# Kernel optimization log

Hardware: AMD Instinct MI355X
Metric: run time of the kernel (lower is better)

Reference implementation:

```python
import jax, jax.numpy as jnp
import numpy as np

R = 8            # receptive_field (hardcoded r=8 in GridProcessing call)
MARGIN = 0.6     # TripletLoss(margin=0.6)
EPS = 1e-8       # F.cosine_similarity eps


def _mine_cords(B, FH, FW):
    """Replicates GridProcessing._prepare for an identity flow field
    G[b, y, x] = ((x + 0.5) / W, (y + 0.5) / H):
    at every cell center, G_xmin = x, G_xmax = x + 1, both inside bounds, and
    [x // r, (x + 1) // r + 1) = {ix}, so the positive window collapses to the
    cell itself -> anchor_cord == positive_cord == (b, ix, iy) for every cell.
    (clip(0, 31) is benign since FH = FW = 32.)
    Negative cords from _prepare are discarded by forward(), so not produced."""
    bs, ys, xs = np.meshgrid(np.arange(B), np.arange(FH), np.arange(FW), indexing='ij')
    idx = np.stack([bs, xs, ys], axis=-1).reshape(-1, 3).astype(np.int32)  # rows: (b, x, y)
    return idx, idx.copy()


def setup_inputs() -> dict:
    key = jax.random.key(0)
    B, C, FH, FW = 16, 1024, 32, 32
    k1, k2 = jax.random.split(key)
    sketch = jax.random.normal(k1, (B, C, FH, FW), dtype=jnp.float32)
    ref = jax.random.normal(k2, (B, C, FH, FW), dtype=jnp.float32)
    a_idx, p_idx = _mine_cords(B, FH, FW)
    return {
        'sketch_query_vectors': sketch,
        'ref_key_vectors': ref,
        'anchor_idx': jnp.asarray(a_idx),
        'positive_idx': jnp.asarray(p_idx),
    }


def reference(sketch_query_vectors, ref_key_vectors, anchor_idx, positive_idx):
    B, C, FH, FW = sketch_query_vectors.shape
    HW = FH * FW
    N = anchor_idx.shape[0]
    na = N // B  # anchor rows are ordered by batch index, na anchors per image

    ax = anchor_idx[:, 1].reshape(B, na)
    ay = anchor_idx[:, 2].reshape(B, na)
    # anchor = sketch[b, :, y, x]  -> (B, na, C)
    a = sketch_query_vectors[jnp.arange(B)[:, None], :, ay, ax]

    # ref_fs.view(c, h*w).permute(1, 0): row-major flatten, flat id = y*W + x
    ref_flat = ref_key_vectors.reshape(B, C, HW).transpose(0, 2, 1)  # (B, HW, C)

    # cosine similarity of every anchor vs every ref position (per batch)
    dots = jnp.einsum('bnc,bmc->bnm', a, ref_flat)          # (B, na, HW)
    a_n = jnp.linalg.norm(a, axis=-1)                        # (B, na)
    r_n = jnp.linalg.norm(ref_flat, axis=-1)                 # (B, HW)
    sim = dots / jnp.maximum(a_n[:, :, None] * r_n[:, None, :], EPS)

    # get_negative_ids: argsort(dist)[:3] -> 3 LOWEST cosine positions;
    # loss uses sum of the 3 anchor-negative cosines (broadcasted cosine sum)
    neg_sum = -jnp.sum(jax.lax.top_k(-sim, 3)[0], axis=-1)   # (B, na)

    # cos(anchor, positive) is just sim at the positive's flat position
    pos_flat = (positive_idx[:, 2] * FW + positive_idx[:, 1]).reshape(B, na)
    cos_ap = jnp.take_along_axis(sim, pos_flat[:, :, None], axis=2)[..., 0]

    # (1 - cos_ap) - (1 - neg_sum) + margin, relu, mean over the single triplet
    losses = jax.nn.relu(neg_sum - cos_ap + MARGIN)          # (B, na)
    return jnp.sum(losses) / (1e-6 + N)
```

## Files before the change

### kernel.cpp

```cpp
#include <hip/hip_runtime.h>
#include <hip/hip_bf16.h>
#include <stdint.h>

#define BATCH 16
#define CDIM  1024
#define FWID  32
#define HW    1024
#define NA    1024
#define NTOT  (BATCH*NA)
#define NCHUNK 16
#define MARGIN 0.6f

typedef __bf16 bf16x8 __attribute__((ext_vector_type(8)));
typedef float  f32x4  __attribute__((ext_vector_type(4)));
typedef unsigned short us4 __attribute__((ext_vector_type(4)));
typedef unsigned short us8 __attribute__((ext_vector_type(8)));
typedef float  f4     __attribute__((ext_vector_type(4)));

template<int OFF>
__device__ __forceinline__ us4 tr_read(uint32_t addr){
  us4 r;
  asm volatile("ds_read_b64_tr_b16 %0, %1 offset:%2" : "=v"(r) : "v"(addr), "n"(OFF));
  return r;
}

__device__ __forceinline__ void gload16(const unsigned short* g, unsigned short* l){
  __builtin_amdgcn_global_load_lds((const __attribute__((address_space(1))) void*)g,
                                   (__attribute__((address_space(3))) void*)l, 16, 0, 0);
}

union FragU  { us4 h[2]; bf16x8 v; };
union FragU8 { us8 u;    bf16x8 v; };

__device__ __forceinline__ void ins3(float& a, float& b, float& c, float v){
  if (v < c){
    c = v;
    if (c < b){ float t=b; b=c; c=t;
      if (b < a){ t=a; a=b; b=t; }
    }
  }
}

#define MFMA __builtin_amdgcn_mfma_f32_16x16x32_bf16

__global__ __launch_bounds__(256)
void convert_transpose(const float* __restrict__ S, const float* __restrict__ R,
                       unsigned short* __restrict__ tS, unsigned short* __restrict__ tR,
                       float* __restrict__ pnorm){
  const int blk = blockIdx.x;
  const int e   = blk >> 11;
  const int b   = (blk >> 7) & 15;
  const int hwT = (blk >> 3) & 15;
  const int cT  = blk & 7;
  const float* src = (e ? R : S) + (size_t)b*CDIM*HW;
  unsigned short* dst = (e ? tR : tS) + (size_t)b*HW*CDIM;

  const int t   = threadIdx.x;
  const int cj  = t & 15;
  const int hwg = t >> 4;
  const int hw0 = hwT*64 + hwg*4;
  const int c0  = cT*128 + cj*8;

  f4 col[8];
  #pragma unroll
  for (int i = 0; i < 8; ++i)
    col[i] = *(const f4*)&src[(size_t)(c0 + i)*HW + hw0];

  float sq0=0.f, sq1=0.f, sq2=0.f, sq3=0.f;
  #pragma unroll
  for (int j = 0; j < 4; ++j){
    us8 pk;
    float sq = 0.f;
    #pragma unroll
    for (int i = 0; i < 8; ++i){
      __hip_bfloat16 h = __float2bfloat16(col[i][j]);
      pk[i] = __builtin_bit_cast(unsigned short, h);
      const float g = __bfloat162float(h);
      sq = fmaf(g, g, sq);
    }
    *(us8*)&dst[(size_t)(hw0 + j)*CDIM + c0] = pk;
    if (j==0) sq0=sq; else if (j==1) sq1=sq; else if (j==2) sq2=sq; else sq3=sq;
  }
  #pragma unroll
  for (int m = 1; m < 16; m <<= 1){
    sq0 += __shfl_xor(sq0, m);
    sq1 += __shfl_xor(sq1, m);
    sq2 += __shfl_xor(sq2, m);
    sq3 += __shfl_xor(sq3, m);
  }
  if (cj == 0){
    f4 o = {sq0, sq1, sq2, sq3};
    *(f4*)&pnorm[((size_t)(e*16 + b)*8 + cT)*HW + hw0] = o;
  }
}

__global__ __launch_bounds__(256)
void norm_reduce(const float* __restrict__ pnorm, float* __restrict__ snorm){
  const int eb = blockIdx.x;
  const int t  = threadIdx.x;
  #pragma unroll
  for (int r = 0; r < 4; ++r){
    const int hw = r*256 + t;
    float a = 0.f;
    #pragma unroll
    for (int ct = 0; ct < 8; ++ct)
      a += pnorm[((size_t)eb*8 + ct)*HW + hw];
    snorm[(size_t)eb*HW + hw] = sqrtf(a);
  }
}

__global__ __launch_bounds__(512, 2)
void fused_gemm_top3_v5(const unsigned short* __restrict__ tS,
                        const unsigned short* __restrict__ tR,
                        const float* __restrict__ snorm,
                        const int*   __restrict__ anchor,
                        const int*   __restrict__ posidx,
                        float* __restrict__ wtop,
                        float* __restrict__ wpos)
{
  __shared__ unsigned short stage[49152];
  __shared__ int   p_lds[256], q_lds[256];
  __shared__ float nAs[256], nBs[256];

  const int t = threadIdx.x;
  const uint32_t bid = blockIdx.x;
  const uint32_t L = (bid & 7u)*32u + (bid >> 3);
  const int b  = L >> 4;
  const int ni = (L >> 2) & 3;
  const int mi = L & 3;

  const unsigned short* SbT = tS + (size_t)b*HW*CDIM;
  const unsigned short* RbT = tR + (size_t)b*HW*CDIM;

  if (t < 256){
    const int n_g = ni*256 + t;
    const int* ap = anchor + (size_t)(b*NA + n_g)*3;
    const int* pp = posidx + (size_t)(b*NA + n_g)*3;
    const int pv = ap[2]*FWID + ap[1];
    p_lds[t] = pv;
    q_lds[t] = pp[2]*FWID + pp[1];
    nAs[t] = 1.0f / snorm[(size_t)b*HW + pv];
  } else {
    nBs[t-256] = 1.0f / snorm[(size_t)(BATCH + b)*HW + mi*256 + (t-256)];
  }
  __syncthreads();

  const int l  = t & 63;
  const int w  = t >> 6;
  const int wr = w >> 2, wc = w & 3;

  const int gkc = (l&3) ^ ((l>>3)&3);
  const int r0  = w*32 + (l>>2);
  const int r1  = r0 + 16;
  const unsigned short* gA0 = SbT + (size_t)p_lds[r0]*CDIM + gkc*8;
  const unsigned short* gA1 = SbT + (size_t)p_lds[r1]*CDIM + gkc*8;
  const unsigned short* gB0 = RbT + (size_t)(mi*256 + r0)*CDIM + gkc*8;
  const unsigned short* gB1 = RbT + (size_t)(mi*256 + r1)*CDIM + gkc*8;
  unsigned short* lA = &stage[w*1024];
  unsigned short* lB = &stage[24576 + w*1024];

  const int fbase = (l&15)*32 + (((l>>4) ^ ((l>>1)&3))*8);
  const int abase = wr*4096 + fbase;
  const int bbase = 24576 + wc*2048 + fbase;

  f32x4 acc[8][4];
  #pragma unroll
  for (int i=0;i<8;i++){
    #pragma unroll
    for (int j=0;j<4;j++){ f32x4 z = {0.f,0.f,0.f,0.f}; acc[i][j] = z; }
  }

  auto stage_fn = [&](int bo, int kt){
    const int ko = kt*32;
    gload16(gA0 + ko, lA + bo);
    gload16(gA1 + ko, lA + bo + 512);
    gload16(gB0 + ko, lB + bo);
    gload16(gB1 + ko, lB + bo + 512);
  };

  auto compute = [&](int bo){
    FragU8 Bf[4], Af[8];
    #pragma unroll
    for (int fb=0; fb<4; ++fb) Bf[fb].u = *(const us8*)&stage[bbase + bo + fb*512];
    #pragma unroll
    for (int fa=0; fa<8; ++fa) Af[fa].u = *(const us8*)&stage[abase + bo + fa*512];
    #pragma unroll
    for (int fa=0; fa<8; ++fa){
      #pragma unroll
      for (int fb=0; fb<4; ++fb)
        acc[fa][fb] = MFMA(Af[fa].v, Bf[fb].v, acc[fa][fb], 0,0,0);
    }
  };

  stage_fn(0, 0);
  stage_fn(8192, 1);
  int oc = 0, on = 8192, on2 = 16384;
  for (int kt = 0; kt < 32; ++kt){
    if (kt < 31) asm volatile("s_waitcnt vmcnt(4)" ::: "memory");
    else         asm volatile("s_waitcnt vmcnt(0)" ::: "memory");
    asm volatile("s_waitcnt lgkmcnt(0)" ::: "memory");
    __builtin_amdgcn_s_barrier();
    if (kt < 30) stage_fn(on2, kt+2);
    compute(oc);
    const int tmp = oc; oc = on; on = on2; on2 = tmp;
  }

  __syncthreads();

  float* tls = (float*)&stage[0] + (size_t)w*1152;

  float rinv[4];
  #pragma unroll
  for (int fb=0; fb<4; ++fb) rinv[fb] = nBs[wc*64 + fb*16 + (l&15)];

  #pragma unroll
  for (int fa=0; fa<8; ++fa){
    #pragma unroll
    for (int r=0; r<4; ++r){
      const int rg    = (l>>4)*4 + r;
      const int row_l = wr*128 + fa*16 + rg;
      const float ain = nAs[row_l];
      const float v0 = acc[fa][0][r] * ain * rinv[0];
      const float v1 = acc[fa][1][r] * ain * rinv[1];
      const float v2 = acc[fa][2][r] * ain * rinv[2];
      const float v3 = acc[fa][3][r] * ain * rinv[3];

      const int n_g = ni*256 + row_l;
      const int q   = q_lds[row_l];
      const int ql  = q - (mi*256 + wc*64);
      if (ql >= 0 && ql < 64 && (ql & 15) == (l & 15)){
        const int sel = ql >> 4;
        const float pv = sel==0 ? v0 : sel==1 ? v1 : sel==2 ? v2 : v3;
        wpos[b*NA + n_g] = pv;
      }

      float x=1e30f, y=1e30f, z=1e30f;
      ins3(x,y,z,v0); ins3(x,y,z,v1); ins3(x,y,z,v2); ins3(x,y,z,v3);
      f4 tr = {x, y, z, 0.f};
      *(f4*)(tls + (rg*17 + (l&15))*4) = tr;
    }
    asm volatile("s_waitcnt lgkmcnt(0)" ::: "memory");
    __builtin_amdgcn_sched_barrier(0);

    {
      const int rr = l >> 2;
      const float* rbp = tls + (rr*17 + (l&3)*4)*4;
      const f4 t0 = *(const f4*)(rbp);
      const f4 t1 = *(const f4*)(rbp + 4);
      const f4 t2 = *(const f4*)(rbp + 8);
      const f4 t3 = *(const f4*)(rbp + 12);
      float x = t0[0], y = t0[1], z = t0[2];
      ins3(x,y,z,t1[0]); ins3(x,y,z,t1[1]); ins3(x,y,z,t1[2]);
      ins3(x,y,z,t2[0]); ins3(x,y,z,t2[1]); ins3(x,y,z,t2[2]);
      ins3(x,y,z,t3[0]); ins3(x,y,z,t3[1]); ins3(x,y,z,t3[2]);
      #pragma unroll
      for (int m=1; m<4; m<<=1){
        const float ox = __shfl_xor(x, m);
        const float oy = __shfl_xor(y, m);
        const float oz = __shfl_xor(z, m);
        ins3(x,y,z,ox); ins3(x,y,z,oy); ins3(x,y,z,oz);
      }
      if ((l & 3) == 0){
        const int n_g = ni*256 + wr*128 + fa*16 + rr;
        float* dst = wtop + ((size_t)(b*NA + n_g)*NCHUNK + (mi*4 + wc))*3;
        dst[0]=x; dst[1]=y; dst[2]=z;
      }
    }
    asm volatile("s_waitcnt lgkmcnt(0)" ::: "memory");
    __builtin_amdgcn_sched_barrier(0);
  }
}

__global__ __launch_bounds__(256)
void fused_gemm_top3_v1(const float* __restrict__ sketch,
                        const float* __restrict__ refk,
                        const int*   __restrict__ anchor,
                        const int*   __restrict__ posidx,
                        float* __restrict__ wtop,
                        float* __restrict__ wpos)
{
  __shared__ union {
    unsigned short stage[16384];
    struct { float nA[16][128]; float nB[16][128]; } nrm;
  } sh;
  __shared__ int   p_lds[128];
  __shared__ float nA2[128], nB2[128];

  const int t = threadIdx.x;
  const uint32_t bid = blockIdx.x;
  const uint32_t L = (bid & 7u)*128u + (bid >> 3);
  const int b  = L >> 6;
  const int ni = (L >> 3) & 7;
  const int mi = L & 7;

  const float* Sb = sketch + (size_t)b*CDIM*HW;
  const float* Rb = refk   + (size_t)b*CDIM*HW;

  if (t < 128){
    const int n_g = ni*128 + t;
    const int* ap = anchor + (size_t)(b*NA + n_g)*3;
    p_lds[t] = ap[2]*FWID + ap[1];
  }
  __syncthreads();
  const int p0 = p_lds[0];
  int okf = 1;
  if (t < 128) okf = (p_lds[t] == p0 + t);
  const int contig = __syncthreads_and(okf);

  const int colg = (t & 15)*8;
  const int rowg = t >> 4;
  const int mbase = mi*128;

  const int l  = t & 63;
  const int w  = t >> 6;
  const int wr = w >> 1, wc = w & 1;
  const uint32_t sh_base = (uint32_t)(uintptr_t)&sh.stage[0];
  const uint32_t laneA = ((uint32_t)(l>>4))*2048u + (uint32_t)wr*512u + (uint32_t)(l&15)*8u;
  const uint32_t laneB = ((uint32_t)(l>>4))*2048u + (uint32_t)wc*512u + (uint32_t)(l&15)*8u;
  const int off0 = ((rowg>>2)*8 + (colg>>4))*64 + (rowg&3)*16 + (colg&15);

  f32x4 acc[4][4];
  #pragma unroll
  for (int i=0;i<4;i++){
    #pragma unroll
    for (int j=0;j<4;j++){ f32x4 z = {0.f,0.f,0.f,0.f}; acc[i][j] = z; }
  }

  float sqA[8] = {0,0,0,0,0,0,0,0};
  float sqB[8] = {0,0,0,0,0,0,0,0};
  f4 ra[4], rb[4];

  auto load_tile = [&](int kt){
    const int c0 = kt*32 + rowg;
    const float* SA = Sb + (size_t)c0*HW;
    const float* RB = Rb + (size_t)c0*HW + mbase + colg;
    if (contig){
      const float* pA = SA + p0 + colg;
      ra[0] = *(const f4*)(pA);
      ra[1] = *(const f4*)(pA + 4);
      ra[2] = *(const f4*)(pA + 16*HW);
      ra[3] = *(const f4*)(pA + 16*HW + 4);
    } else {
      float* raf = (float*)ra;
      #pragma unroll
      for (int i=0;i<8;i++){
        const int pc = p_lds[colg + i];
        raf[i]   = SA[pc];
        raf[8+i] = SA[16*HW + pc];
      }
    }
    rb[0] = *(const f4*)(RB);
    rb[1] = *(const f4*)(RB + 4);
    rb[2] = *(const f4*)(RB + 16*HW);
    rb[3] = *(const f4*)(RB + 16*HW + 4);
  };

  auto cvt_store = [&](int buf){
    const float* raf = (const float*)ra;
    const float* rbf = (const float*)rb;
    us8 pk;
    #pragma unroll
    for (int i=0;i<8;i++){
      __hip_bfloat16 h = __float2bfloat16(raf[i]);
      pk[i] = __builtin_bit_cast(unsigned short, h);
      const float g = __bfloat162float(h);
      sqA[i] = fmaf(g, g, sqA[i]);
    }
    *(us8*)&sh.stage[buf*4096 + off0] = pk;
    #pragma unroll
    for (int i=0;i<8;i++){
      __hip_bfloat16 h = __float2bfloat16(raf[8+i]);
      pk[i] = __builtin_bit_cast(unsigned short, h);
      const float g = __bfloat162float(h);
      sqA[i] = fmaf(g, g, sqA[i]);
    }
    *(us8*)&sh.stage[buf*4096 + off0 + 2048] = pk;
    #pragma unroll
    for (int i=0;i<8;i++){
      __hip_bfloat16 h = __float2bfloat16(rbf[i]);
      pk[i] = __builtin_bit_cast(unsigned short, h);
      const float g = __bfloat162float(h);
      sqB[i] = fmaf(g, g, sqB[i]);
    }
    *(us8*)&sh.stage[8192 + buf*4096 + off0] = pk;
    #pragma unroll
    for (int i=0;i<8;i++){
      __hip_bfloat16 h = __float2bfloat16(rbf[8+i]);
      pk[i] = __builtin_bit_cast(unsigned short, h);
      const float g = __bfloat162float(h);
      sqB[i] = fmaf(g, g, sqB[i]);
    }
    *(us8*)&sh.stage[8192 + buf*4096 + off0 + 2048] = pk;
  };

  auto compute = [&](int buf){
    const uint32_t aaddr = sh_base + (uint32_t)buf*8192u + laneA;
    const uint32_t baddr = sh_base + 16384u + (uint32_t)buf*8192u + laneB;
    FragU A0,A1,A2,A3,B0,B1,B2,B3;
    A0.h[0]=tr_read<0>(aaddr);    A0.h[1]=tr_read<1024>(aaddr);
    A1.h[0]=tr_read<128>(aaddr);  A1.h[1]=tr_read<1152>(aaddr);
    A2.h[0]=tr_read<256>(aaddr);  A2.h[1]=tr_read<1280>(aaddr);
    A3.h[0]=tr_read<384>(aaddr);  A3.h[1]=tr_read<1408>(aaddr);
    B0.h[0]=tr_read<0>(baddr);    B0.h[1]=tr_read<1024>(baddr);
    B1.h[0]=tr_read<128>(baddr);  B1.h[1]=tr_read<1152>(baddr);
    B2.h[0]=tr_read<256>(baddr);  B2.h[1]=tr_read<1280>(baddr);
    B3.h[0]=tr_read<384>(baddr);  B3.h[1]=tr_read<1408>(baddr);
    asm volatile("s_waitcnt lgkmcnt(0)" ::: "memory");
    __builtin_amdgcn_sched_barrier(0);
    acc[0][0]=MFMA(A0.v,B0.v,acc[0][0],0,0,0);
    acc[0][1]=MFMA(A0.v,B1.v,acc[0][1],0,0,0);
    acc[0][2]=MFMA(A0.v,B2.v,acc[0][2],0,0,0);
    acc[0][3]=MFMA(A0.v,B3.v,acc[0][3],0,0,0);
    acc[1][0]=MFMA(A1.v,B0.v,acc[1][0],0,0,0);
    acc[1][1]=MFMA(A1.v,B1.v,acc[1][1],0,0,0);
    acc[1][2]=MFMA(A1.v,B2.v,acc[1][2],0,0,0);
    acc[1][3]=MFMA(A1.v,B3.v,acc[1][3],0,0,0);
    acc[2][0]=MFMA(A2.v,B0.v,acc[2][0],0,0,0);
    acc[2][1]=MFMA(A2.v,B1.v,acc[2][1],0,0,0);
    acc[2][2]=MFMA(A2.v,B2.v,acc[2][2],0,0,0);
    acc[2][3]=MFMA(A2.v,B3.v,acc[2][3],0,0,0);
    acc[3][0]=MFMA(A3.v,B0.v,acc[3][0],0,0,0);
    acc[3][1]=MFMA(A3.v,B1.v,acc[3][1],0,0,0);
    acc[3][2]=MFMA(A3.v,B2.v,acc[3][2],0,0,0);
    acc[3][3]=MFMA(A3.v,B3.v,acc[3][3],0,0,0);
  };

  load_tile(0);
  cvt_store(0);
  __syncthreads();
  int buf = 0;
  for (int kt = 0; kt < 32; ++kt){
    if (kt < 31) load_tile(kt+1);
    compute(buf);
    if (kt < 31) cvt_store(buf^1);
    __syncthreads();
    buf ^= 1;
  }

  #pragma unroll
  for (int i=0;i<8;i++) sh.nrm.nA[rowg][colg+i] = sqA[i];
  #pragma unroll
  for (int i=0;i<8;i++) sh.nrm.nB[rowg][colg+i] = sqB[i];
  __syncthreads();
  if (t < 128){
    float s = 0.f;
    #pragma unroll
    for (int r=0;r<16;r++) s += sh.nrm.nA[r][t];
    nA2[t] = s;
  } else {
    const int c2 = t - 128;
    float s = 0.f;
    #pragma unroll
    for (int r=0;r<16;r++) s += sh.nrm.nB[r][c2];
    nB2[c2] = s;
  }
  __syncthreads();

  float rncol[4];
  #pragma unroll
  for (int nf=0;nf<4;nf++) rncol[nf] = sqrtf(nB2[wc*64 + nf*16 + (l&15)]);

  #pragma unroll
  for (int mf=0; mf<4; ++mf){
    #pragma unroll
    for (int r=0; r<4; ++r){
      const int row_l = wr*64 + mf*16 + (l>>4)*4 + r;
      const int n_g   = ni*128 + row_l;
      const float an  = sqrtf(nA2[row_l]);
      const float v0 = acc[mf][0][r] / fmaxf(an*rncol[0], 1e-8f);
      const float v1 = acc[mf][1][r] / fmaxf(an*rncol[1], 1e-8f);
      const float v2 = acc[mf][2][r] / fmaxf(an*rncol[2], 1e-8f);
      const float v3 = acc[mf][3][r] / fmaxf(an*rncol[3], 1e-8f);

      const int* pp = posidx + (size_t)(b*NA + n_g)*3;
      const int q  = pp[2]*FWID + pp[1];
      const int ql = q - (mbase + wc*64);
      if (ql >= 0 && ql < 64 && (ql & 15) == (l & 15)){
        const int sel = ql >> 4;
        const float pv = sel==0 ? v0 : sel==1 ? v1 : sel==2 ? v2 : v3;
        wpos[b*NA + n_g] = pv;
      }

      float x=1e30f, y=1e30f, z=1e30f;
      ins3(x,y,z,v0); ins3(x,y,z,v1); ins3(x,y,z,v2); ins3(x,y,z,v3);
      #pragma unroll
      for (int m=1; m<16; m<<=1){
        const float ox = __shfl_xor(x, m);
        const float oy = __shfl_xor(y, m);
        const float oz = __shfl_xor(z, m);
        ins3(x,y,z,ox); ins3(x,y,z,oy); ins3(x,y,z,oz);
      }
      if ((l & 15) == 0){
        float* dst = wtop + ((size_t)(b*NA + n_g)*NCHUNK + (mi*2 + wc))*3;
        dst[0]=x; dst[1]=y; dst[2]=z;
      }
    }
  }
}

__global__ __launch_bounds__(256)
void merge_top3(const float* __restrict__ wtop, const float* __restrict__ wpos,
                float* __restrict__ partial){
  __shared__ float red[256];
  const int id = blockIdx.x*256 + threadIdx.x;
  const float* src = wtop + (size_t)id*(NCHUNK*3);
  float x=1e30f, y=1e30f, z=1e30f;
  #pragma unroll
  for (int i=0;i<NCHUNK*3;i++) ins3(x,y,z, src[i]);
  const float loss = fmaxf((x+y+z) - wpos[id] + MARGIN, 0.0f);
  red[threadIdx.x] = loss;
  __syncthreads();
  for (int s=128; s>0; s>>=1){
    if (threadIdx.x < s) red[threadIdx.x] += red[threadIdx.x+s];
    __syncthreads();
  }
  if (threadIdx.x == 0) partial[blockIdx.x] = red[0];
}

__global__ void final_sum(const float* __restrict__ partial, float* __restrict__ out){
  float v = partial[threadIdx.x];
  #pragma unroll
  for (int off=32; off>0; off>>=1) v += __shfl_down(v, off);
  if (threadIdx.x == 0) out[0] = v / (1e-6f + (float)NTOT);
}

extern "C" void kernel_launch(void* const* d_in, const int* in_sizes, int n_in,
                              void* d_out, int out_size, void* d_ws, size_t ws_size,
                              hipStream_t stream){
  const float* sketch = (const float*)d_in[0];
  const float* refk   = (const float*)d_in[1];
  const int*   anchor = (const int*)d_in[2];
  const int*   posidx = (const int*)d_in[3];
  float* out = (float*)d_out;

  float* wtop    = (float*)d_ws;
  float* wpos    = wtop + (size_t)NTOT*NCHUNK*3;
  float* partial = wpos + NTOT;
  unsigned short* tS = (unsigned short*)(partial + 256);
  unsigned short* tR = tS + (size_t)BATCH*HW*CDIM;
  float* pnorm = (float*)(tR + (size_t)BATCH*HW*CDIM);
  float* snorm = pnorm + (size_t)32*8*1024;
  const size_t need = (size_t)((char*)(snorm + 32*1024) - (char*)d_ws);

  if (ws_size >= need){
    convert_transpose<<<dim3(4096), dim3(256), 0, stream>>>(sketch, refk, tS, tR, pnorm);
    norm_reduce<<<dim3(32), dim3(256), 0, stream>>>(pnorm, snorm);
    fused_gemm_top3_v5<<<dim3(256), dim3(512), 0, stream>>>(tS, tR, snorm, anchor, posidx, wtop, wpos);
  } else {
    fused_gemm_top3_v1<<<dim3(1024), dim3(256), 0, stream>>>(sketch, refk, anchor, posidx, wtop, wpos);
  }
  merge_top3<<<dim3(64), dim3(256), 0, stream>>>(wtop, wpos, partial);
  final_sum<<<dim3(1), dim3(64), 0, stream>>>(partial, out);
}
```

Before: 104.4 us.

## Deepen GEMM K-tile to 64 with double buffering and halve transpose grid

The GEMM main loop now stages 64-wide K tiles instead of 32, uses two LDS buffers instead of three, and uses a new XOR swizzle over 8 chunks. Each stage is computed as two half-steps, with s_setprio raised around the MFMA bursts. The convert/transpose kernel now handles two 128-channel slabs per block, halving the grid so each thread has more loads in flight. The aim is fewer barriers per K and better latency hiding. The cost is more LDS per block (64K shorts), which may limit occupancy, and a full vmcnt(0) wait each iteration.

```diff
diff --git a/kernel.cpp b/kernel.cpp
--- a/kernel.cpp
+++ b/kernel.cpp
@@ -44,14 +44,14 @@
 #define MFMA __builtin_amdgcn_mfma_f32_16x16x32_bf16
 
 __global__ __launch_bounds__(256)
-void convert_transpose(const float* __restrict__ S, const float* __restrict__ R,
-                       unsigned short* __restrict__ tS, unsigned short* __restrict__ tR,
-                       float* __restrict__ pnorm){
+void convert_transpose3(const float* __restrict__ S, const float* __restrict__ R,
+                        unsigned short* __restrict__ tS, unsigned short* __restrict__ tR,
+                        float* __restrict__ pnorm){
   const int blk = blockIdx.x;
-  const int e   = blk >> 11;
-  const int b   = (blk >> 7) & 15;
-  const int hwT = (blk >> 3) & 15;
-  const int cT  = blk & 7;
+  const int e   = blk >> 10;
+  const int b   = (blk >> 6) & 15;
+  const int hwT = (blk >> 2) & 15;
+  const int cP  = blk & 3;
   const float* src = (e ? R : S) + (size_t)b*CDIM*HW;
   unsigned short* dst = (e ? tR : tS) + (size_t)b*HW*CDIM;
 
@@ -59,38 +59,60 @@
   const int cj  = t & 15;
   const int hwg = t >> 4;
   const int hw0 = hwT*64 + hwg*4;
-  const int c0  = cT*128 + cj*8;
-
-  f4 col[8];
+  const int cA  = cP*256 + cj*8;
+  const int cB  = cA + 128;
+
+  f4 colA[8], colB[8];
   #pragma unroll
   for (int i = 0; i < 8; ++i)
-    col[i] = *(const f4*)&src[(size_t)(c0 + i)*HW + hw0];
-
-  float sq0=0.f, sq1=0.f, sq2=0.f, sq3=0.f;
+    colA[i] = *(const f4*)&src[(size_t)(cA + i)*HW + hw0];
+  #pragma unroll
+  for (int i = 0; i < 8; ++i)
+    colB[i] = *(const f4*)&src[(size_t)(cB + i)*HW + hw0];
+
+  float sqa[4] = {0.f,0.f,0.f,0.f};
+  float sqb[4] = {0.f,0.f,0.f,0.f};
   #pragma unroll
   for (int j = 0; j < 4; ++j){
     us8 pk;
     float sq = 0.f;
     #pragma unroll
     for (int i = 0; i < 8; ++i){
-      __hip_bfloat16 h = __float2bfloat16(col[i][j]);
+      __hip_bfloat16 h = __float2bfloat16(colA[i][j]);
       pk[i] = __builtin_bit_cast(unsigned short, h);
       const float g = __bfloat162float(h);
       sq = fmaf(g, g, sq);
     }
-    *(us8*)&dst[(size_t)(hw0 + j)*CDIM + c0] = pk;
-    if (j==0) sq0=sq; else if (j==1) sq1=sq; else if (j==2) sq2=sq; else sq3=sq;
+    *(us8*)&dst[(size_t)(hw0 + j)*CDIM + cA] = pk;
+    sqa[j] = sq;
+  }
+  #pragma unroll
+  for (int j = 0; j < 4; ++j){
+    us8 pk;
+    float sq = 0.f;
+    #pragma unroll
+    for (int i = 0; i < 8; ++i){
+      __hip_bfloat16 h = __float2bfloat16(colB[i][j]);
+      pk[i] = __builtin_bit_cast(unsigned short, h);
+      const float g = __bfloat162float(h);
+      sq = fmaf(g, g, sq);
+    }
+    *(us8*)&dst[(size_t)(hw0 + j)*CDIM + cB] = pk;
+    sqb[j] = sq;
   }
   #pragma unroll
   for (int m = 1; m < 16; m <<= 1){
-    sq0 += __shfl_xor(sq0, m);
-    sq1 += __shfl_xor(sq1, m);
-    sq2 += __shfl_xor(sq2, m);
-    sq3 += __shfl_xor(sq3, m);
+    #pragma unroll
+    for (int j = 0; j < 4; ++j){
+      sqa[j] += __shfl_xor(sqa[j], m);
+      sqb[j] += __shfl_xor(sqb[j], m);
+    }
   }
   if (cj == 0){
-    f4 o = {sq0, sq1, sq2, sq3};
-    *(f4*)&pnorm[((size_t)(e*16 + b)*8 + cT)*HW + hw0] = o;
+    f4 oa = {sqa[0], sqa[1], sqa[2], sqa[3]};
+    f4 ob = {sqb[0], sqb[1], sqb[2], sqb[3]};
+    *(f4*)&pnorm[((size_t)(e*16 + b)*8 + cP*2    )*HW + hw0] = oa;
+    *(f4*)&pnorm[((size_t)(e*16 + b)*8 + cP*2 + 1)*HW + hw0] = ob;
   }
 }
 
@@ -110,7 +132,7 @@
 }
 
 __global__ __launch_bounds__(512, 2)
-void fused_gemm_top3_v5(const unsigned short* __restrict__ tS,
+void fused_gemm_top3_v9(const unsigned short* __restrict__ tS,
                         const unsigned short* __restrict__ tR,
                         const float* __restrict__ snorm,
                         const int*   __restrict__ anchor,
@@ -118,7 +140,7 @@
                         float* __restrict__ wtop,
                         float* __restrict__ wpos)
 {
-  __shared__ unsigned short stage[49152];
+  __shared__ unsigned short stage[65536];
   __shared__ int   p_lds[256], q_lds[256];
   __shared__ float nAs[256], nBs[256];
 
@@ -149,19 +171,22 @@
   const int w  = t >> 6;
   const int wr = w >> 2, wc = w & 3;
 
-  const int gkc = (l&3) ^ ((l>>3)&3);
-  const int r0  = w*32 + (l>>2);
-  const int r1  = r0 + 16;
-  const unsigned short* gA0 = SbT + (size_t)p_lds[r0]*CDIM + gkc*8;
-  const unsigned short* gA1 = SbT + (size_t)p_lds[r1]*CDIM + gkc*8;
-  const unsigned short* gB0 = RbT + (size_t)(mi*256 + r0)*CDIM + gkc*8;
-  const unsigned short* gB1 = RbT + (size_t)(mi*256 + r1)*CDIM + gkc*8;
-  unsigned short* lA = &stage[w*1024];
-  unsigned short* lB = &stage[24576 + w*1024];
-
-  const int fbase = (l&15)*32 + (((l>>4) ^ ((l>>1)&3))*8);
-  const int abase = wr*4096 + fbase;
-  const int bbase = 24576 + wc*2048 + fbase;
+  const int gkc = (l&7) ^ ((l>>3)&7);
+  const unsigned short* gA[4];
+  const unsigned short* gB[4];
+  #pragma unroll
+  for (int i = 0; i < 4; ++i){
+    const int row = w*32 + i*8 + (l>>3);
+    gA[i] = SbT + (size_t)p_lds[row]*CDIM + gkc*8;
+    gB[i] = RbT + (size_t)(mi*256 + row)*CDIM + gkc*8;
+  }
+  unsigned short* lA = &stage[w*2048];
+  unsigned short* lB = &stage[32768 + w*2048];
+
+  const int fb0 = (l&15)*64 + (((l>>4)    ) ^ (l&7))*8;
+  const int fb1 = (l&15)*64 + (((l>>4) + 4) ^ (l&7))*8;
+  const int abase = wr*8192;
+  const int bbase = 32768 + wc*4096;
 
   f32x4 acc[8][4];
   #pragma unroll
@@ -170,43 +195,44 @@
     for (int j=0;j<4;j++){ f32x4 z = {0.f,0.f,0.f,0.f}; acc[i][j] = z; }
   }
 
-  auto stage_fn = [&](int bo, int kt){
-    const int ko = kt*32;
-    gload16(gA0 + ko, lA + bo);
-    gload16(gA1 + ko, lA + bo + 512);
-    gload16(gB0 + ko, lB + bo);
-    gload16(gB1 + ko, lB + bo + 512);
+  auto stage8 = [&](int bo, int kt){
+    const int ko = kt*64;
+    #pragma unroll
+    for (int i = 0; i < 4; ++i){
+      gload16(gA[i] + ko, lA + bo + i*512);
+      gload16(gB[i] + ko, lB + bo + i*512);
+    }
   };
 
-  auto compute = [&](int bo){
+  auto half = [&](int bo, int fbh){
     FragU8 Bf[4], Af[8];
     #pragma unroll
-    for (int fb=0; fb<4; ++fb) Bf[fb].u = *(const us8*)&stage[bbase + bo + fb*512];
-    #pragma unroll
-    for (int fa=0; fa<8; ++fa) Af[fa].u = *(const us8*)&stage[abase + bo + fa*512];
+    for (int fb=0; fb<4; ++fb) Bf[fb].u = *(const us8*)&stage[bbase + bo + fb*1024 + fbh];
+    #pragma unroll
+    for (int fa=0; fa<8; ++fa) Af[fa].u = *(const us8*)&stage[abase + bo + fa*1024 + fbh];
+    __builtin_amdgcn_s_setprio(1);
     #pragma unroll
     for (int fa=0; fa<8; ++fa){
       #pragma unroll
       for (int fb=0; fb<4; ++fb)
         acc[fa][fb] = MFMA(Af[fa].v, Bf[fb].v, acc[fa][fb], 0,0,0);
     }
+    __builtin_amdgcn_s_setprio(0);
   };
 
-  stage_fn(0, 0);
-  stage_fn(8192, 1);
-  int oc = 0, on = 8192, on2 = 16384;
-  for (int kt = 0; kt < 32; ++kt){
-    if (kt < 31) asm volatile("s_waitcnt vmcnt(4)" ::: "memory");
-    else         asm volatile("s_waitcnt vmcnt(0)" ::: "memory");
-    asm volatile("s_waitcnt lgkmcnt(0)" ::: "memory");
+  stage8(0, 0);
+  int bo = 0;
+  for (int kt = 0; kt < 16; ++kt){
+    asm volatile("s_waitcnt vmcnt(0)" ::: "memory");
     __builtin_amdgcn_s_barrier();
-    if (kt < 30) stage_fn(on2, kt+2);
-    compute(oc);
-    const int tmp = oc; oc = on; on = on2; on2 = tmp;
-  }
-
-  __syncthreads();
-
+    __builtin_amdgcn_sched_barrier(0);
+    if (kt < 15) stage8(bo ^ 16384, kt+1);
+    half(bo, fb0);
+    half(bo, fb1);
+    bo ^= 16384;
+  }
+
+  __syncthreads();
   float* tls = (float*)&stage[0] + (size_t)w*1152;
 
   float rinv[4];
@@ -543,9 +569,9 @@
   const size_t need = (size_t)((char*)(snorm + 32*1024) - (char*)d_ws);
 
   if (ws_size >= need){
-    convert_transpose<<<dim3(4096), dim3(256), 0, stream>>>(sketch, refk, tS, tR, pnorm);
+    convert_transpose3<<<dim3(2048), dim3(256), 0, stream>>>(sketch, refk, tS, tR, pnorm);
     norm_reduce<<<dim3(32), dim3(256), 0, stream>>>(pnorm, snorm);
-    fused_gemm_top3_v5<<<dim3(256), dim3(512), 0, stream>>>(tS, tR, snorm, anchor, posidx, wtop, wpos);
+    fused_gemm_top3_v9<<<dim3(256), dim3(512), 0, stream>>>(tS, tR, snorm, anchor, posidx, wtop, wpos);
   } else {
     fused_gemm_top3_v1<<<dim3(1024), dim3(256), 0, stream>>>(sketch, refk, anchor, posidx, wtop, wpos);
   }
```

Result: faster. 97.25 us (-6.8%).
